# Optimization experiments

Measured on AMD Instinct MI355X. Metric: run time of the kernel, lower is better.

The kernel has to match this reference:

```python
import jax, jax.numpy as jnp
import numpy as np

B, T, C, H = 4096, 32, 180, 6
HD = C // H  # 30
EPS = 1e-5

def _ln(x, g, b):
    mu = jnp.mean(x, axis=-1, keepdims=True)
    var = jnp.mean(jnp.square(x - mu), axis=-1, keepdims=True)
    return (x - mu) * jax.lax.rsqrt(var + EPS) * g + b

def setup_inputs() -> dict:
    key = jax.random.key(0)
    ks = jax.random.split(key, 12)
    s_in = 1.0 / np.sqrt(C)
    s_ff = 1.0 / np.sqrt(4 * C)
    return {
        "x": jax.random.normal(ks[0], (B, T, C), jnp.float32),
        "wq": jax.random.normal(ks[1], (H, C, HD), jnp.float32) * s_in,
        "wk": jax.random.normal(ks[2], (H, C, HD), jnp.float32) * s_in,
        "wv": jax.random.normal(ks[3], (H, C, HD), jnp.float32) * s_in,
        "g1": jnp.ones((C,), jnp.float32),
        "be1": jnp.zeros((C,), jnp.float32),
        "g2": jnp.ones((C,), jnp.float32),
        "be2": jnp.zeros((C,), jnp.float32),
        "w1": jax.random.normal(ks[4], (C, 4 * C), jnp.float32) * s_in,
        "b1": jnp.zeros((4 * C,), jnp.float32),
        "w2": jax.random.normal(ks[5], (4 * C, C), jnp.float32) * s_ff,
        "b2": jnp.zeros((C,), jnp.float32),
    }

def reference(x, wq, wk, wv, g1, be1, g2, be2, w1, b1, w2, b2):
    Bv, Tv, Cv = x.shape
    h = _ln(x, g1, be1)
    # batched multi-head QKV (replaces per-head Python loop)
    q = jnp.einsum('btc,hcd->bhtd', h, wq)
    k = jnp.einsum('btc,hcd->bhtd', h, wk)
    v = jnp.einsum('btc,hcd->bhtd', h, wv)
    scores = jnp.einsum('bhtd,bhsd->bhts', q, k) * (HD ** -0.5)
    mask = jnp.tril(jnp.ones((Tv, Tv), bool))
    scores = jnp.where(mask, scores, -jnp.inf)
    attn = jax.nn.softmax(scores, axis=-1)  # dropout off (eval)
    out = jnp.einsum('bhts,bhsd->bhtd', attn, v)
    out = jnp.transpose(out, (0, 2, 1, 3)).reshape(Bv, Tv, Cv)  # concat heads
    x = x + out
    h2 = _ln(x, g2, be2)
    mlp = jax.nn.relu(h2 @ w1 + b1) @ w2 + b2  # dropout off (eval)
    return x + mlp
```

## Files before the change

### kernel.cpp

```cpp
#include <hip/hip_runtime.h>

typedef __attribute__((ext_vector_type(8))) short short8;
typedef __attribute__((ext_vector_type(4))) float f32x4;
typedef unsigned short ushort_t;
typedef unsigned int u32;
typedef unsigned long long u64;

#define MFMA16(a,b,c) __builtin_amdgcn_mfma_f32_16x16x32_bf16((a),(b),(c),0,0,0)

__device__ __forceinline__ ushort_t f2bf(float f){
  union { float f; u32 u; } v; v.f = f;
  u32 r = v.u + 0x7fffu + ((v.u >> 16) & 1u);
  return (ushort_t)(r >> 16);
}
__device__ __forceinline__ float bf2f(ushort_t h){
  union { u32 u; float f; } v; v.u = ((u32)h) << 16; return v.f;
}

#define WQKV_ELEMS (576*192)
#define W1T_ELEMS  (768*192)
#define W2T_ELEMS  (192*768)

__global__ void prep_weights(const float* __restrict__ wq, const float* __restrict__ wk,
                             const float* __restrict__ wv, const float* __restrict__ w1,
                             const float* __restrict__ w2, ushort_t* __restrict__ ws){
  ushort_t* wqkv = ws;
  ushort_t* w1t = ws + WQKV_ELEMS;
  ushort_t* w2t = w1t + W1T_ELEMS;
  int tid = blockIdx.x * blockDim.x + threadIdx.x;
  int stride = gridDim.x * blockDim.x;
  for (int i = tid; i < WQKV_ELEMS; i += stride){
    int k = i % 192; int row = i / 192;
    int d = row & 31; int m = (row >> 5) % 3; int h = row / 96;
    float v = 0.f;
    if (d < 30 && k < 180){
      const float* W = (m == 0) ? wq : ((m == 1) ? wk : wv);
      v = W[(h*180 + k)*30 + d];
    }
    wqkv[i] = f2bf(v);
  }
  for (int i = tid; i < W1T_ELEMS; i += stride){
    int c = i % 192; int n = i / 192;
    float v = (n < 720 && c < 180) ? w1[c*720 + n] : 0.f;
    w1t[i] = f2bf(v);
  }
  for (int i = tid; i < W2T_ELEMS; i += stride){
    int c4 = i % 768; int n = i / 768;
    float v = (n < 180 && c4 < 720) ? w2[c4*180 + n] : 0.f;
    w2t[i] = f2bf(v);
  }
}

__global__ __launch_bounds__(256, 2)
void attn_kernel(const float* __restrict__ x, const float* __restrict__ g1,
                 const float* __restrict__ be1, const ushort_t* __restrict__ wqkv,
                 float* __restrict__ xout){
  __shared__ ushort_t h_lds[64*200];
  __shared__ ushort_t q_s[4][32*40];
  __shared__ ushort_t k_s[4][32*40];
  __shared__ ushort_t v_s[4][32*40];
  __shared__ float    l_s[4][32];
  __shared__ ushort_t att[64*196];

  int tid = threadIdx.x;
  int wave = tid >> 6;
  int lane = tid & 63;
  int quad = lane >> 4;
  int c16 = lane & 15;
  long block0 = (long)blockIdx.x * 64;

  for (int i = tid; i < 64*200/2; i += 256) ((u32*)h_lds)[i] = 0u;
  __syncthreads();

  int row = tid >> 2, sub = tid & 3;
  const float* xrow = x + (block0 + row) * 180;
  float s1 = 0.f, s2 = 0.f;
  #pragma unroll
  for (int i = 0; i < 45; i++){
    float v = xrow[sub*45 + i];
    s1 += v; s2 += v*v;
  }
  s1 += __shfl_xor(s1, 1); s1 += __shfl_xor(s1, 2);
  s2 += __shfl_xor(s2, 1); s2 += __shfl_xor(s2, 2);
  float mu = s1 * (1.f/180.f);
  float rstd = rsqrtf(s2 * (1.f/180.f) - mu*mu + 1e-5f);
  #pragma unroll
  for (int i = 0; i < 45; i++){
    int col = sub*45 + i;
    h_lds[row*200 + col] = f2bf((xrow[col] - mu) * rstd * g1[col] + be1[col]);
  }
  __syncthreads();

  int bb = wave & 1;
  int hg = wave >> 1;
  ushort_t* qs = q_s[wave]; ushort_t* ks = k_s[wave]; ushort_t* vs = v_s[wave];
  float* ls = l_s[wave];

  for (int hh = 0; hh < 3; hh++){
    int head = hg*3 + hh;
    const ushort_t* wbase = wqkv + head*3*32*192;
    f32x4 acc[2][6];
    #pragma unroll
    for (int i=0;i<2;i++){
      #pragma unroll
      for (int j=0;j<6;j++) acc[i][j] = (f32x4)0.f;
    }
    #pragma unroll
    for (int kk = 0; kk < 6; kk++){
      int k0 = kk*32;
      short8 a[2];
      #pragma unroll
      for (int mt=0; mt<2; mt++)
        a[mt] = *(const short8*)(h_lds + (bb*32 + mt*16 + c16)*200 + k0 + quad*8);
      short8 b[6];
      #pragma unroll
      for (int nb=0; nb<6; nb++)
        b[nb] = *(const short8*)(wbase + ((nb>>1)*32 + (nb&1)*16 + c16)*192 + k0 + quad*8);
      #pragma unroll
      for (int mt=0; mt<2; mt++){
        #pragma unroll
        for (int nb=0; nb<6; nb++)
          acc[mt][nb] = MFMA16(a[mt], b[nb], acc[mt][nb]);
      }
    }
    #pragma unroll
    for (int mt=0; mt<2; mt++){
      #pragma unroll
      for (int nt=0; nt<2; nt++){
        #pragma unroll
        for (int r=0;r<4;r++){
          int t = mt*16 + quad*4 + r;
          int d = nt*16 + c16;
          qs[t*40 + d] = f2bf(acc[mt][nt][r]);
          ks[t*40 + d] = f2bf(acc[mt][2+nt][r]);
        }
        u32 p0 = (u32)f2bf(acc[mt][4+nt][0]) | ((u32)f2bf(acc[mt][4+nt][1]) << 16);
        u32 p1 = (u32)f2bf(acc[mt][4+nt][2]) | ((u32)f2bf(acc[mt][4+nt][3]) << 16);
        u64 pv = (u64)p0 | ((u64)p1 << 32);
        *(u64*)(vs + (nt*16 + c16)*40 + mt*16 + quad*4) = pv;
      }
    }
    f32x4 sacc[2][2];
    #pragma unroll
    for (int i=0;i<2;i++){ sacc[i][0] = (f32x4)0.f; sacc[i][1] = (f32x4)0.f; }
    short8 aq[2], bk[2];
    #pragma unroll
    for (int mt=0;mt<2;mt++) aq[mt] = *(const short8*)(qs + (mt*16 + c16)*40 + quad*8);
    #pragma unroll
    for (int nt=0;nt<2;nt++) bk[nt] = *(const short8*)(ks + (nt*16 + c16)*40 + quad*8);
    #pragma unroll
    for (int mt=0;mt<2;mt++){
      #pragma unroll
      for (int nt=0;nt<2;nt++)
        sacc[mt][nt] = MFMA16(aq[mt], bk[nt], sacc[mt][nt]);
    }
    const float scl = 0.18257418583505537f;
    #pragma unroll
    for (int mt=0;mt<2;mt++){
      #pragma unroll
      for (int r=0;r<4;r++){
        int t = mt*16 + quad*4 + r;
        float v0 = sacc[mt][0][r] * scl; if (c16 > t) v0 = -1e30f;
        float v1 = sacc[mt][1][r] * scl; if (16 + c16 > t) v1 = -1e30f;
        float m = fmaxf(v0, v1);
        m = fmaxf(m, __shfl_xor(m, 1));
        m = fmaxf(m, __shfl_xor(m, 2));
        m = fmaxf(m, __shfl_xor(m, 4));
        m = fmaxf(m, __shfl_xor(m, 8));
        float e0 = __expf(v0 - m), e1 = __expf(v1 - m);
        float sum = e0 + e1;
        sum += __shfl_xor(sum, 1); sum += __shfl_xor(sum, 2);
        sum += __shfl_xor(sum, 4); sum += __shfl_xor(sum, 8);
        qs[t*40 + c16] = f2bf(e0);
        qs[t*40 + 16 + c16] = f2bf(e1);
        if (c16 == 0) ls[t] = sum;
      }
    }
    f32x4 oacc[2][2];
    #pragma unroll
    for (int i=0;i<2;i++){ oacc[i][0] = (f32x4)0.f; oacc[i][1] = (f32x4)0.f; }
    short8 av[2], bp[2];
    #pragma unroll
    for (int dt=0;dt<2;dt++) av[dt] = *(const short8*)(vs + (dt*16 + c16)*40 + quad*8);
    #pragma unroll
    for (int tt=0;tt<2;tt++) bp[tt] = *(const short8*)(qs + (tt*16 + c16)*40 + quad*8);
    #pragma unroll
    for (int dt=0;dt<2;dt++){
      #pragma unroll
      for (int tt=0;tt<2;tt++)
        oacc[dt][tt] = MFMA16(av[dt], bp[tt], oacc[dt][tt]);
    }
    #pragma unroll
    for (int dt=0;dt<2;dt++){
      #pragma unroll
      for (int tt=0;tt<2;tt++){
        int t = tt*16 + c16;
        float linv = 1.f / ls[t];
        u32 p0 = (u32)f2bf(oacc[dt][tt][0]*linv) | ((u32)f2bf(oacc[dt][tt][1]*linv) << 16);
        u32 p1 = (u32)f2bf(oacc[dt][tt][2]*linv) | ((u32)f2bf(oacc[dt][tt][3]*linv) << 16);
        u64 pp = (u64)p0 | ((u64)p1 << 32);
        *(u64*)(att + (bb*32 + t)*196 + head*32 + dt*16 + quad*4) = pp;
      }
    }
  }

  __syncthreads();
  #pragma unroll
  for (int i = 0; i < 45; i++){
    int col = sub*45 + i;
    int hd = col / 30;
    int d = col - hd*30;
    float a = bf2f(att[row*196 + hd*32 + d]);
    xout[(block0 + row)*180 + col] = xrow[col] + a;
  }
}

__global__ __launch_bounds__(256, 2)
void mlp_kernel(const float* __restrict__ g2, const float* __restrict__ be2,
                const float* __restrict__ b1, const float* __restrict__ b2,
                const ushort_t* __restrict__ w1t, const ushort_t* __restrict__ w2t,
                float* __restrict__ xio){
  __shared__ ushort_t h2[64*200];
  __shared__ ushort_t act[64*200];
  int tid = threadIdx.x;
  int wave = tid >> 6, lane = tid & 63;
  int quad = lane >> 4, c16 = lane & 15;
  long row0 = (long)blockIdx.x * 64;

  for (int i = tid; i < 64*200/2; i += 256) ((u32*)h2)[i] = 0u;
  __syncthreads();

  int row = tid >> 2, sub = tid & 3;
  const float* xr = xio + (row0 + row)*180;
  float s1 = 0.f, s2 = 0.f;
  #pragma unroll
  for (int i = 0; i < 45; i++){
    float v = xr[sub*45 + i];
    s1 += v; s2 += v*v;
  }
  s1 += __shfl_xor(s1, 1); s1 += __shfl_xor(s1, 2);
  s2 += __shfl_xor(s2, 1); s2 += __shfl_xor(s2, 2);
  float mu = s1 * (1.f/180.f);
  float rstd = rsqrtf(s2 * (1.f/180.f) - mu*mu + 1e-5f);
  #pragma unroll
  for (int i = 0; i < 45; i++){
    int col = sub*45 + i;
    h2[row*200 + col] = f2bf((xr[col] - mu) * rstd * g2[col] + be2[col]);
  }
  __syncthreads();

  f32x4 outacc[4][3];
  #pragma unroll
  for (int i=0;i<4;i++){
    #pragma unroll
    for (int j=0;j<3;j++) outacc[i][j] = (f32x4)0.f;
  }

  for (int ch = 0; ch < 4; ch++){
    f32x4 aacc[3][4];
    #pragma unroll
    for (int i=0;i<3;i++){
      #pragma unroll
      for (int j=0;j<4;j++) aacc[i][j] = (f32x4)0.f;
    }
    #pragma unroll
    for (int kk=0; kk<6; kk++){
      int k0 = kk*32;
      short8 aw[3];
      #pragma unroll
      for (int mi=0; mi<3; mi++)
        aw[mi] = *(const short8*)(w1t + (size_t)(ch*192 + (wave*3+mi)*16 + c16)*192 + k0 + quad*8);
      short8 bh[4];
      #pragma unroll
      for (int tt=0; tt<4; tt++)
        bh[tt] = *(const short8*)(h2 + (tt*16 + c16)*200 + k0 + quad*8);
      #pragma unroll
      for (int mi=0; mi<3; mi++){
        #pragma unroll
        for (int tt=0; tt<4; tt++)
          aacc[mi][tt] = MFMA16(aw[mi], bh[tt], aacc[mi][tt]);
      }
    }
    __syncthreads();
    #pragma unroll
    for (int mi=0; mi<3; mi++){
      int nb = ch*192 + (wave*3+mi)*16 + quad*4;
      f32x4 bias = (f32x4)0.f;
      if (nb < 720) bias = *(const f32x4*)(b1 + nb);
      #pragma unroll
      for (int tt=0; tt<4; tt++){
        int token = tt*16 + c16;
        float v0 = fmaxf(aacc[mi][tt][0] + bias[0], 0.f);
        float v1 = fmaxf(aacc[mi][tt][1] + bias[1], 0.f);
        float v2 = fmaxf(aacc[mi][tt][2] + bias[2], 0.f);
        float v3 = fmaxf(aacc[mi][tt][3] + bias[3], 0.f);
        u32 p0 = (u32)f2bf(v0) | ((u32)f2bf(v1) << 16);
        u32 p1 = (u32)f2bf(v2) | ((u32)f2bf(v3) << 16);
        u64 pp = (u64)p0 | ((u64)p1 << 32);
        *(u64*)(act + token*200 + (wave*3+mi)*16 + quad*4) = pp;
      }
    }
    __syncthreads();
    #pragma unroll
    for (int kk=0; kk<6; kk++){
      int k0 = kk*32;
      short8 aa[4];
      #pragma unroll
      for (int mt=0; mt<4; mt++)
        aa[mt] = *(const short8*)(act + (mt*16 + c16)*200 + k0 + quad*8);
      short8 bw[3];
      #pragma unroll
      for (int ntl=0; ntl<3; ntl++)
        bw[ntl] = *(const short8*)(w2t + (size_t)(wave*48 + ntl*16 + c16)*768 + ch*192 + k0 + quad*8);
      #pragma unroll
      for (int mt=0; mt<4; mt++){
        #pragma unroll
        for (int ntl=0; ntl<3; ntl++)
          outacc[mt][ntl] = MFMA16(aa[mt], bw[ntl], outacc[mt][ntl]);
      }
    }
  }
  #pragma unroll
  for (int ntl=0; ntl<3; ntl++){
    int nout = wave*48 + ntl*16 + c16;
    if (nout < 180){
      float bias2 = b2[nout];
      #pragma unroll
      for (int mt=0; mt<4; mt++){
        #pragma unroll
        for (int r=0;r<4;r++){
          long token = row0 + mt*16 + quad*4 + r;
          long idx = token*180 + nout;
          xio[idx] = xio[idx] + outacc[mt][ntl][r] + bias2;
        }
      }
    }
  }
}

extern "C" void kernel_launch(void* const* d_in, const int* in_sizes, int n_in,
                              void* d_out, int out_size, void* d_ws, size_t ws_size,
                              hipStream_t stream) {
  const float* x   = (const float*)d_in[0];
  const float* wq  = (const float*)d_in[1];
  const float* wk  = (const float*)d_in[2];
  const float* wv  = (const float*)d_in[3];
  const float* g1  = (const float*)d_in[4];
  const float* be1 = (const float*)d_in[5];
  const float* g2  = (const float*)d_in[6];
  const float* be2 = (const float*)d_in[7];
  const float* w1  = (const float*)d_in[8];
  const float* b1  = (const float*)d_in[9];
  const float* w2  = (const float*)d_in[10];
  const float* b2  = (const float*)d_in[11];
  ushort_t* ws   = (ushort_t*)d_ws;
  ushort_t* wqkv = ws;
  ushort_t* w1t  = ws + WQKV_ELEMS;
  ushort_t* w2t  = w1t + W1T_ELEMS;
  float* out = (float*)d_out;

  prep_weights<<<256, 256, 0, stream>>>(wq, wk, wv, w1, w2, ws);
  attn_kernel<<<2048, 256, 0, stream>>>(x, g1, be1, wqkv, out);
  mlp_kernel<<<2048, 256, 0, stream>>>(g2, be2, b1, b2, w1t, w2t, out);
}
```

Baseline: 502.8 us.

## Restructure attention and MLP kernels with coalesced float4 I/O and one batch per block

The attention kernel now handles one batch (32 tokens) per block with 6 waves, one head per wave, and the MLP kernel processes 32 tokens per block with higher occupancy. Both kernels load x as coalesced float4, stage it in LDS as bf16, and compute LayerNorm from LDS. Cross-lane reductions move to DPP, and softmax normalisation is applied before the PV product. The MLP output goes through LDS for a coalesced float4 residual write. The LayerNorm input is now rounded to bf16 before the statistics are taken, and the MLP delta is rounded to bf16 before it is added, which adds precision loss.

```diff
diff --git a/kernel.cpp b/kernel.cpp
--- a/kernel.cpp
+++ b/kernel.cpp
@@ -15,6 +15,33 @@
 }
 __device__ __forceinline__ float bf2f(ushort_t h){
   union { u32 u; float f; } v; v.u = ((u32)h) << 16; return v.f;
+}
+
+template<int CTRL>
+__device__ __forceinline__ float dpp_add(float x){
+  union { float f; int i; } a, b;
+  a.f = x;
+  b.i = __builtin_amdgcn_update_dpp(a.i, a.i, CTRL, 0xF, 0xF, false);
+  return x + b.f;
+}
+template<int CTRL>
+__device__ __forceinline__ float dpp_max(float x){
+  union { float f; int i; } a, b;
+  a.f = x;
+  b.i = __builtin_amdgcn_update_dpp(a.i, a.i, CTRL, 0xF, 0xF, false);
+  return fmaxf(x, b.f);
+}
+__device__ __forceinline__ float red16_add(float x){
+  x = dpp_add<0xB1>(x); x = dpp_add<0x4E>(x); x = dpp_add<0x141>(x); x = dpp_add<0x140>(x);
+  return x;
+}
+__device__ __forceinline__ float red16_max(float x){
+  x = dpp_max<0xB1>(x); x = dpp_max<0x4E>(x); x = dpp_max<0x141>(x); x = dpp_max<0x140>(x);
+  return x;
+}
+__device__ __forceinline__ float red8_add(float x){
+  x = dpp_add<0xB1>(x); x = dpp_add<0x4E>(x); x = dpp_add<0x141>(x);
+  return x;
 }
 
 #define WQKV_ELEMS (576*192)
@@ -51,244 +78,267 @@
   }
 }
 
-__global__ __launch_bounds__(256, 2)
+#define HXS 200
+#define ATS 196
+__global__ __launch_bounds__(384, 3)
 void attn_kernel(const float* __restrict__ x, const float* __restrict__ g1,
                  const float* __restrict__ be1, const ushort_t* __restrict__ wqkv,
                  float* __restrict__ xout){
-  __shared__ ushort_t h_lds[64*200];
-  __shared__ ushort_t q_s[4][32*40];
-  __shared__ ushort_t k_s[4][32*40];
-  __shared__ ushort_t v_s[4][32*40];
-  __shared__ float    l_s[4][32];
-  __shared__ ushort_t att[64*196];
+  __shared__ ushort_t hx[32*HXS];
+  __shared__ ushort_t att[32*ATS];
+  __shared__ ushort_t qp[6][32*40];
+  __shared__ ushort_t kv[6][32*40];
 
   int tid = threadIdx.x;
-  int wave = tid >> 6;
-  int lane = tid & 63;
-  int quad = lane >> 4;
-  int c16 = lane & 15;
-  long block0 = (long)blockIdx.x * 64;
-
-  for (int i = tid; i < 64*200/2; i += 256) ((u32*)h_lds)[i] = 0u;
-  __syncthreads();
-
-  int row = tid >> 2, sub = tid & 3;
-  const float* xrow = x + (block0 + row) * 180;
-  float s1 = 0.f, s2 = 0.f;
-  #pragma unroll
-  for (int i = 0; i < 45; i++){
-    float v = xrow[sub*45 + i];
-    s1 += v; s2 += v*v;
-  }
-  s1 += __shfl_xor(s1, 1); s1 += __shfl_xor(s1, 2);
-  s2 += __shfl_xor(s2, 1); s2 += __shfl_xor(s2, 2);
-  float mu = s1 * (1.f/180.f);
-  float rstd = rsqrtf(s2 * (1.f/180.f) - mu*mu + 1e-5f);
-  #pragma unroll
-  for (int i = 0; i < 45; i++){
-    int col = sub*45 + i;
-    h_lds[row*200 + col] = f2bf((xrow[col] - mu) * rstd * g1[col] + be1[col]);
-  }
-  __syncthreads();
-
-  int bb = wave & 1;
-  int hg = wave >> 1;
-  ushort_t* qs = q_s[wave]; ushort_t* ks = k_s[wave]; ushort_t* vs = v_s[wave];
-  float* ls = l_s[wave];
-
-  for (int hh = 0; hh < 3; hh++){
-    int head = hg*3 + hh;
-    const ushort_t* wbase = wqkv + head*3*32*192;
+  int wave = tid >> 6, lane = tid & 63;
+  int quad = lane >> 4, c16 = lane & 15;
+  long base = (long)blockIdx.x * 5760;
+
+  #pragma unroll
+  for (int it = 0; it < 4; it++){
+    int idx = it*384 + tid;
+    if (idx < 1440){
+      f32x4 v = *(const f32x4*)(x + base + (long)idx*4);
+      int row = (int)(((u32)idx * 745655u) >> 25);
+      int col = idx - row*45;
+      u32 p0 = (u32)f2bf(v.x) | ((u32)f2bf(v.y) << 16);
+      u32 p1 = (u32)f2bf(v.z) | ((u32)f2bf(v.w) << 16);
+      *(u64*)(hx + row*HXS + col*4) = (u64)p0 | ((u64)p1 << 32);
+    } else {
+      int p = idx - 1440;
+      int row = (p*21846) >> 16;
+      int c = p - row*3;
+      *(u64*)(hx + row*HXS + 180 + c*4) = 0ull;
+    }
+  }
+  __syncthreads();
+
+  if (tid < 256){
+    int row = tid >> 3, sub = tid & 7;
+    int c0 = sub*23;
+    float s1 = 0.f, s2 = 0.f;
+    #pragma unroll
+    for (int i = 0; i < 23; i++){
+      int c = c0 + i;
+      if (c < 180){ float v = bf2f(hx[row*HXS + c]); s1 += v; s2 += v*v; }
+    }
+    s1 = red8_add(s1); s2 = red8_add(s2);
+    float mu = s1 * (1.f/180.f);
+    float rstd = rsqrtf(s2 * (1.f/180.f) - mu*mu + 1e-5f);
+    #pragma unroll
+    for (int i = 0; i < 23; i++){
+      int c = c0 + i;
+      if (c < 180){
+        float v = bf2f(hx[row*HXS + c]);
+        hx[row*HXS + c] = f2bf((v - mu)*rstd*g1[c] + be1[c]);
+      }
+    }
+  }
+  __syncthreads();
+
+  {
+    const ushort_t* wbase = wqkv + wave*3*32*192;
+    ushort_t* qs = qp[wave];
+    ushort_t* ks = kv[wave];
+
     f32x4 acc[2][6];
     #pragma unroll
-    for (int i=0;i<2;i++){
-      #pragma unroll
-      for (int j=0;j<6;j++) acc[i][j] = (f32x4)0.f;
-    }
+    for (int i = 0; i < 2; i++)
+      #pragma unroll
+      for (int j = 0; j < 6; j++) acc[i][j] = (f32x4)0.f;
     #pragma unroll
     for (int kk = 0; kk < 6; kk++){
       int k0 = kk*32;
       short8 a[2];
       #pragma unroll
-      for (int mt=0; mt<2; mt++)
-        a[mt] = *(const short8*)(h_lds + (bb*32 + mt*16 + c16)*200 + k0 + quad*8);
+      for (int mt = 0; mt < 2; mt++)
+        a[mt] = *(const short8*)(hx + (mt*16 + c16)*HXS + k0 + quad*8);
       short8 b[6];
       #pragma unroll
-      for (int nb=0; nb<6; nb++)
+      for (int nb = 0; nb < 6; nb++)
         b[nb] = *(const short8*)(wbase + ((nb>>1)*32 + (nb&1)*16 + c16)*192 + k0 + quad*8);
       #pragma unroll
-      for (int mt=0; mt<2; mt++){
+      for (int mt = 0; mt < 2; mt++)
         #pragma unroll
-        for (int nb=0; nb<6; nb++)
+        for (int nb = 0; nb < 6; nb++)
           acc[mt][nb] = MFMA16(a[mt], b[nb], acc[mt][nb]);
-      }
-    }
-    #pragma unroll
-    for (int mt=0; mt<2; mt++){
-      #pragma unroll
-      for (int nt=0; nt<2; nt++){
+    }
+    #pragma unroll
+    for (int mt = 0; mt < 2; mt++)
+      #pragma unroll
+      for (int nt = 0; nt < 2; nt++)
         #pragma unroll
-        for (int r=0;r<4;r++){
+        for (int r = 0; r < 4; r++){
           int t = mt*16 + quad*4 + r;
           int d = nt*16 + c16;
           qs[t*40 + d] = f2bf(acc[mt][nt][r]);
           ks[t*40 + d] = f2bf(acc[mt][2+nt][r]);
         }
-        u32 p0 = (u32)f2bf(acc[mt][4+nt][0]) | ((u32)f2bf(acc[mt][4+nt][1]) << 16);
-        u32 p1 = (u32)f2bf(acc[mt][4+nt][2]) | ((u32)f2bf(acc[mt][4+nt][3]) << 16);
-        u64 pv = (u64)p0 | ((u64)p1 << 32);
-        *(u64*)(vs + (nt*16 + c16)*40 + mt*16 + quad*4) = pv;
-      }
-    }
     f32x4 sacc[2][2];
     #pragma unroll
-    for (int i=0;i<2;i++){ sacc[i][0] = (f32x4)0.f; sacc[i][1] = (f32x4)0.f; }
+    for (int i = 0; i < 2; i++){ sacc[i][0] = (f32x4)0.f; sacc[i][1] = (f32x4)0.f; }
     short8 aq[2], bk[2];
     #pragma unroll
-    for (int mt=0;mt<2;mt++) aq[mt] = *(const short8*)(qs + (mt*16 + c16)*40 + quad*8);
-    #pragma unroll
-    for (int nt=0;nt<2;nt++) bk[nt] = *(const short8*)(ks + (nt*16 + c16)*40 + quad*8);
-    #pragma unroll
-    for (int mt=0;mt<2;mt++){
-      #pragma unroll
-      for (int nt=0;nt<2;nt++)
+    for (int mt = 0; mt < 2; mt++) aq[mt] = *(const short8*)(qs + (mt*16 + c16)*40 + quad*8);
+    #pragma unroll
+    for (int nt = 0; nt < 2; nt++) bk[nt] = *(const short8*)(ks + (nt*16 + c16)*40 + quad*8);
+    #pragma unroll
+    for (int mt = 0; mt < 2; mt++)
+      #pragma unroll
+      for (int nt = 0; nt < 2; nt++)
         sacc[mt][nt] = MFMA16(aq[mt], bk[nt], sacc[mt][nt]);
-    }
     const float scl = 0.18257418583505537f;
     #pragma unroll
-    for (int mt=0;mt<2;mt++){
-      #pragma unroll
-      for (int r=0;r<4;r++){
+    for (int mt = 0; mt < 2; mt++)
+      #pragma unroll
+      for (int r = 0; r < 4; r++){
         int t = mt*16 + quad*4 + r;
         float v0 = sacc[mt][0][r] * scl; if (c16 > t) v0 = -1e30f;
         float v1 = sacc[mt][1][r] * scl; if (16 + c16 > t) v1 = -1e30f;
-        float m = fmaxf(v0, v1);
-        m = fmaxf(m, __shfl_xor(m, 1));
-        m = fmaxf(m, __shfl_xor(m, 2));
-        m = fmaxf(m, __shfl_xor(m, 4));
-        m = fmaxf(m, __shfl_xor(m, 8));
+        float m = red16_max(fmaxf(v0, v1));
         float e0 = __expf(v0 - m), e1 = __expf(v1 - m);
-        float sum = e0 + e1;
-        sum += __shfl_xor(sum, 1); sum += __shfl_xor(sum, 2);
-        sum += __shfl_xor(sum, 4); sum += __shfl_xor(sum, 8);
-        qs[t*40 + c16] = f2bf(e0);
-        qs[t*40 + 16 + c16] = f2bf(e1);
-        if (c16 == 0) ls[t] = sum;
-      }
-    }
+        float s = red16_add(e0 + e1);
+        float inv = 1.f / s;
+        qs[t*40 + c16]      = f2bf(e0 * inv);
+        qs[t*40 + 16 + c16] = f2bf(e1 * inv);
+      }
+    #pragma unroll
+    for (int mt = 0; mt < 2; mt++)
+      #pragma unroll
+      for (int nt = 0; nt < 2; nt++){
+        u32 p0 = (u32)f2bf(acc[mt][4+nt][0]) | ((u32)f2bf(acc[mt][4+nt][1]) << 16);
+        u32 p1 = (u32)f2bf(acc[mt][4+nt][2]) | ((u32)f2bf(acc[mt][4+nt][3]) << 16);
+        *(u64*)(ks + (nt*16 + c16)*40 + mt*16 + quad*4) = (u64)p0 | ((u64)p1 << 32);
+      }
     f32x4 oacc[2][2];
     #pragma unroll
-    for (int i=0;i<2;i++){ oacc[i][0] = (f32x4)0.f; oacc[i][1] = (f32x4)0.f; }
+    for (int i = 0; i < 2; i++){ oacc[i][0] = (f32x4)0.f; oacc[i][1] = (f32x4)0.f; }
     short8 av[2], bp[2];
     #pragma unroll
-    for (int dt=0;dt<2;dt++) av[dt] = *(const short8*)(vs + (dt*16 + c16)*40 + quad*8);
-    #pragma unroll
-    for (int tt=0;tt<2;tt++) bp[tt] = *(const short8*)(qs + (tt*16 + c16)*40 + quad*8);
-    #pragma unroll
-    for (int dt=0;dt<2;dt++){
-      #pragma unroll
-      for (int tt=0;tt<2;tt++)
+    for (int dt = 0; dt < 2; dt++) av[dt] = *(const short8*)(ks + (dt*16 + c16)*40 + quad*8);
+    #pragma unroll
+    for (int tt = 0; tt < 2; tt++) bp[tt] = *(const short8*)(qs + (tt*16 + c16)*40 + quad*8);
+    #pragma unroll
+    for (int dt = 0; dt < 2; dt++)
+      #pragma unroll
+      for (int tt = 0; tt < 2; tt++)
         oacc[dt][tt] = MFMA16(av[dt], bp[tt], oacc[dt][tt]);
-    }
-    #pragma unroll
-    for (int dt=0;dt<2;dt++){
-      #pragma unroll
-      for (int tt=0;tt<2;tt++){
-        int t = tt*16 + c16;
-        float linv = 1.f / ls[t];
-        u32 p0 = (u32)f2bf(oacc[dt][tt][0]*linv) | ((u32)f2bf(oacc[dt][tt][1]*linv) << 16);
-        u32 p1 = (u32)f2bf(oacc[dt][tt][2]*linv) | ((u32)f2bf(oacc[dt][tt][3]*linv) << 16);
-        u64 pp = (u64)p0 | ((u64)p1 << 32);
-        *(u64*)(att + (bb*32 + t)*196 + head*32 + dt*16 + quad*4) = pp;
-      }
-    }
-  }
-
-  __syncthreads();
-  #pragma unroll
-  for (int i = 0; i < 45; i++){
-    int col = sub*45 + i;
-    int hd = col / 30;
-    int d = col - hd*30;
-    float a = bf2f(att[row*196 + hd*32 + d]);
-    xout[(block0 + row)*180 + col] = xrow[col] + a;
-  }
-}
-
-__global__ __launch_bounds__(256, 2)
+    #pragma unroll
+    for (int dt = 0; dt < 2; dt++)
+      #pragma unroll
+      for (int tt = 0; tt < 2; tt++){
+        u32 p0 = (u32)f2bf(oacc[dt][tt][0]) | ((u32)f2bf(oacc[dt][tt][1]) << 16);
+        u32 p1 = (u32)f2bf(oacc[dt][tt][2]) | ((u32)f2bf(oacc[dt][tt][3]) << 16);
+        *(u64*)(att + (tt*16 + c16)*ATS + wave*32 + dt*16 + quad*4) = (u64)p0 | ((u64)p1 << 32);
+      }
+  }
+  __syncthreads();
+
+  #pragma unroll
+  for (int it = 0; it < 4; it++){
+    int idx = it*384 + tid;
+    if (idx < 1440){
+      f32x4 v = *(const f32x4*)(x + base + (long)idx*4);
+      int row = (int)(((u32)idx * 745655u) >> 25);
+      int col4 = (idx - row*45)*4;
+      #pragma unroll
+      for (int e = 0; e < 4; e++){
+        int c = col4 + e;
+        int h = (c*4370) >> 17;
+        int d = c - h*30;
+        v[e] += bf2f(att[row*ATS + h*32 + d]);
+      }
+      *(f32x4*)(xout + base + (long)idx*4) = v;
+    }
+  }
+}
+
+__global__ __launch_bounds__(256, 4)
 void mlp_kernel(const float* __restrict__ g2, const float* __restrict__ be2,
                 const float* __restrict__ b1, const float* __restrict__ b2,
                 const ushort_t* __restrict__ w1t, const ushort_t* __restrict__ w2t,
                 float* __restrict__ xio){
-  __shared__ ushort_t h2[64*200];
-  __shared__ ushort_t act[64*200];
+  __shared__ ushort_t h2[32*200];
+  __shared__ ushort_t act[32*200];
   int tid = threadIdx.x;
   int wave = tid >> 6, lane = tid & 63;
   int quad = lane >> 4, c16 = lane & 15;
-  long row0 = (long)blockIdx.x * 64;
-
-  for (int i = tid; i < 64*200/2; i += 256) ((u32*)h2)[i] = 0u;
-  __syncthreads();
-
-  int row = tid >> 2, sub = tid & 3;
-  const float* xr = xio + (row0 + row)*180;
-  float s1 = 0.f, s2 = 0.f;
-  #pragma unroll
-  for (int i = 0; i < 45; i++){
-    float v = xr[sub*45 + i];
-    s1 += v; s2 += v*v;
-  }
-  s1 += __shfl_xor(s1, 1); s1 += __shfl_xor(s1, 2);
-  s2 += __shfl_xor(s2, 1); s2 += __shfl_xor(s2, 2);
-  float mu = s1 * (1.f/180.f);
-  float rstd = rsqrtf(s2 * (1.f/180.f) - mu*mu + 1e-5f);
-  #pragma unroll
-  for (int i = 0; i < 45; i++){
-    int col = sub*45 + i;
-    h2[row*200 + col] = f2bf((xr[col] - mu) * rstd * g2[col] + be2[col]);
-  }
-  __syncthreads();
-
-  f32x4 outacc[4][3];
-  #pragma unroll
-  for (int i=0;i<4;i++){
-    #pragma unroll
-    for (int j=0;j<3;j++) outacc[i][j] = (f32x4)0.f;
-  }
+  long base = (long)blockIdx.x * 5760;
+
+  #pragma unroll
+  for (int it = 0; it < 6; it++){
+    int idx = it*256 + tid;
+    if (idx < 1440){
+      f32x4 v = *(const f32x4*)(xio + base + (long)idx*4);
+      int row = (int)(((u32)idx * 745655u) >> 25);
+      int col = idx - row*45;
+      u32 p0 = (u32)f2bf(v.x) | ((u32)f2bf(v.y) << 16);
+      u32 p1 = (u32)f2bf(v.z) | ((u32)f2bf(v.w) << 16);
+      *(u64*)(act + row*200 + col*4) = (u64)p0 | ((u64)p1 << 32);
+    }
+  }
+  __syncthreads();
+
+  {
+    int row = tid >> 3, sub = tid & 7;
+    int c0 = sub*23;
+    float s1 = 0.f, s2 = 0.f;
+    #pragma unroll
+    for (int i = 0; i < 23; i++){
+      int c = c0 + i;
+      if (c < 180){ float v = bf2f(act[row*200 + c]); s1 += v; s2 += v*v; }
+    }
+    s1 = red8_add(s1); s2 = red8_add(s2);
+    float mu = s1 * (1.f/180.f);
+    float rstd = rsqrtf(s2 * (1.f/180.f) - mu*mu + 1e-5f);
+    #pragma unroll
+    for (int i = 0; i < 23; i++){
+      int c = c0 + i;
+      if (c < 180){
+        float v = bf2f(act[row*200 + c]);
+        h2[row*200 + c] = f2bf((v - mu)*rstd*g2[c] + be2[c]);
+      }
+    }
+    if (sub < 6) ((u32*)h2)[row*100 + 90 + sub] = 0u;
+  }
+  __syncthreads();
+
+  f32x4 outacc[2][3];
+  #pragma unroll
+  for (int i = 0; i < 2; i++)
+    #pragma unroll
+    for (int j = 0; j < 3; j++) outacc[i][j] = (f32x4)0.f;
 
   for (int ch = 0; ch < 4; ch++){
-    f32x4 aacc[3][4];
-    #pragma unroll
-    for (int i=0;i<3;i++){
-      #pragma unroll
-      for (int j=0;j<4;j++) aacc[i][j] = (f32x4)0.f;
-    }
-    #pragma unroll
-    for (int kk=0; kk<6; kk++){
+    f32x4 aacc[3][2];
+    #pragma unroll
+    for (int i = 0; i < 3; i++){ aacc[i][0] = (f32x4)0.f; aacc[i][1] = (f32x4)0.f; }
+    #pragma unroll
+    for (int kk = 0; kk < 6; kk++){
       int k0 = kk*32;
       short8 aw[3];
       #pragma unroll
-      for (int mi=0; mi<3; mi++)
+      for (int mi = 0; mi < 3; mi++)
         aw[mi] = *(const short8*)(w1t + (size_t)(ch*192 + (wave*3+mi)*16 + c16)*192 + k0 + quad*8);
-      short8 bh[4];
-      #pragma unroll
-      for (int tt=0; tt<4; tt++)
+      short8 bh[2];
+      #pragma unroll
+      for (int tt = 0; tt < 2; tt++)
         bh[tt] = *(const short8*)(h2 + (tt*16 + c16)*200 + k0 + quad*8);
       #pragma unroll
-      for (int mi=0; mi<3; mi++){
+      for (int mi = 0; mi < 3; mi++)
         #pragma unroll
-        for (int tt=0; tt<4; tt++)
+        for (int tt = 0; tt < 2; tt++)
           aacc[mi][tt] = MFMA16(aw[mi], bh[tt], aacc[mi][tt]);
-      }
     }
     __syncthreads();
     #pragma unroll
-    for (int mi=0; mi<3; mi++){
-      int nb = ch*192 + (wave*3+mi)*16 + quad*4;
+    for (int mi = 0; mi < 3; mi++){
+      int nrel = (wave*3+mi)*16 + quad*4;
+      int nabs = ch*192 + nrel;
       f32x4 bias = (f32x4)0.f;
-      if (nb < 720) bias = *(const f32x4*)(b1 + nb);
-      #pragma unroll
-      for (int tt=0; tt<4; tt++){
+      if (nabs < 720) bias = *(const f32x4*)(b1 + nabs);
+      #pragma unroll
+      for (int tt = 0; tt < 2; tt++){
         int token = tt*16 + c16;
         float v0 = fmaxf(aacc[mi][tt][0] + bias[0], 0.f);
         float v1 = fmaxf(aacc[mi][tt][1] + bias[1], 0.f);
@@ -296,44 +346,55 @@
         float v3 = fmaxf(aacc[mi][tt][3] + bias[3], 0.f);
         u32 p0 = (u32)f2bf(v0) | ((u32)f2bf(v1) << 16);
         u32 p1 = (u32)f2bf(v2) | ((u32)f2bf(v3) << 16);
-        u64 pp = (u64)p0 | ((u64)p1 << 32);
-        *(u64*)(act + token*200 + (wave*3+mi)*16 + quad*4) = pp;
+        *(u64*)(act + token*200 + nrel) = (u64)p0 | ((u64)p1 << 32);
       }
     }
     __syncthreads();
     #pragma unroll
-    for (int kk=0; kk<6; kk++){
+    for (int kk = 0; kk < 6; kk++){
       int k0 = kk*32;
-      short8 aa[4];
-      #pragma unroll
-      for (int mt=0; mt<4; mt++)
+      short8 aa[2];
+      #pragma unroll
+      for (int mt = 0; mt < 2; mt++)
         aa[mt] = *(const short8*)(act + (mt*16 + c16)*200 + k0 + quad*8);
       short8 bw[3];
       #pragma unroll
-      for (int ntl=0; ntl<3; ntl++)
+      for (int ntl = 0; ntl < 3; ntl++)
         bw[ntl] = *(const short8*)(w2t + (size_t)(wave*48 + ntl*16 + c16)*768 + ch*192 + k0 + quad*8);
       #pragma unroll
-      for (int mt=0; mt<4; mt++){
+      for (int mt = 0; mt < 2; mt++)
         #pragma unroll
-        for (int ntl=0; ntl<3; ntl++)
+        for (int ntl = 0; ntl < 3; ntl++)
           outacc[mt][ntl] = MFMA16(aa[mt], bw[ntl], outacc[mt][ntl]);
-      }
-    }
-  }
-  #pragma unroll
-  for (int ntl=0; ntl<3; ntl++){
-    int nout = wave*48 + ntl*16 + c16;
-    if (nout < 180){
-      float bias2 = b2[nout];
-      #pragma unroll
-      for (int mt=0; mt<4; mt++){
-        #pragma unroll
-        for (int r=0;r<4;r++){
-          long token = row0 + mt*16 + quad*4 + r;
-          long idx = token*180 + nout;
-          xio[idx] = xio[idx] + outacc[mt][ntl][r] + bias2;
-        }
-      }
+    }
+  }
+  __syncthreads();
+  #pragma unroll
+  for (int ntl = 0; ntl < 3; ntl++){
+    int n = wave*48 + ntl*16 + c16;
+    #pragma unroll
+    for (int mt = 0; mt < 2; mt++)
+      #pragma unroll
+      for (int r = 0; r < 4; r++){
+        int token = mt*16 + quad*4 + r;
+        act[token*200 + n] = f2bf(outacc[mt][ntl][r]);
+      }
+  }
+  __syncthreads();
+  #pragma unroll
+  for (int it = 0; it < 6; it++){
+    int idx = it*256 + tid;
+    if (idx < 1440){
+      f32x4 v = *(const f32x4*)(xio + base + (long)idx*4);
+      int row = (int)(((u32)idx * 745655u) >> 25);
+      int col4 = (idx - row*45)*4;
+      f32x4 bb = *(const f32x4*)(b2 + col4);
+      u64 m = *(const u64*)(act + row*200 + col4);
+      v.x += bf2f((ushort_t)(m      & 0xFFFF)) + bb.x;
+      v.y += bf2f((ushort_t)((m>>16) & 0xFFFF)) + bb.y;
+      v.z += bf2f((ushort_t)((m>>32) & 0xFFFF)) + bb.z;
+      v.w += bf2f((ushort_t)((m>>48) & 0xFFFF)) + bb.w;
+      *(f32x4*)(xio + base + (long)idx*4) = v;
     }
   }
 }
@@ -360,6 +421,6 @@
   float* out = (float*)d_out;
 
   prep_weights<<<256, 256, 0, stream>>>(wq, wk, wv, w1, w2, ws);
-  attn_kernel<<<2048, 256, 0, stream>>>(x, g1, be1, wqkv, out);
-  mlp_kernel<<<2048, 256, 0, stream>>>(g2, be2, b1, b2, w1t, w2t, out);
-}
+  attn_kernel<<<4096, 384, 0, stream>>>(x, g1, be1, wqkv, out);
+  mlp_kernel<<<4096, 256, 0, stream>>>(g2, be2, b1, b2, w1t, w2t, out);
+}
```

After: 649.4 us. 29.2% more time.
